# Performance work log

Measured on AMD Instinct MI355X. Metric: run time of the kernel, lower is better.

## Reference

```python
import jax, jax.numpy as jnp
import numpy as np

B, N, D, H = 8, 1024, 768, 12
HD = D // H


def setup_inputs() -> dict:
    key = jax.random.key(0)
    ks = jax.random.split(key, 9)
    s = 1.0 / np.sqrt(D)
    return {
        "x": jax.random.normal(ks[0], (B, N, D), dtype=jnp.float32),
        "Wq": jax.random.normal(ks[1], (D, D), dtype=jnp.float32) * s,
        "bq": jax.random.normal(ks[2], (D,), dtype=jnp.float32) * 0.01,
        "Wk": jax.random.normal(ks[3], (D, D), dtype=jnp.float32) * s,
        "bk": jax.random.normal(ks[4], (D,), dtype=jnp.float32) * 0.01,
        "Wv": jax.random.normal(ks[5], (D, D), dtype=jnp.float32) * s,
        "bv": jax.random.normal(ks[6], (D,), dtype=jnp.float32) * 0.01,
        "Wo": jax.random.normal(ks[7], (D, D), dtype=jnp.float32) * s,
        "bo": jax.random.normal(ks[8], (D,), dtype=jnp.float32) * 0.01,
    }


def reference(x, Wq, bq, Wk, bk, Wv, bv, Wo, bo):
    b, n, d = x.shape
    split = lambda t: t.reshape(b, n, H, HD).transpose(0, 2, 1, 3)  # b h n d
    q = split(x @ Wq + bq)
    k = split(x @ Wk + bk)
    v = split(x @ Wv + bv)
    energy = jnp.einsum('bhqd,bhkd->bhqk', q, k)
    # NOTE: module scales AFTER softmax by sqrt(emb_size) (not head_dim) -- faithful.
    att = jax.nn.softmax(energy, axis=-1) / jnp.sqrt(jnp.float32(D)).astype(x.dtype)
    out = jnp.einsum('bhqk,bhkd->bhqd', att, v)
    out = out.transpose(0, 2, 1, 3).reshape(b, n, d)
    return out @ Wo + bo
```

## Files before the change

kernel.cpp:

```cpp
#include <hip/hip_runtime.h>

#define B_  8
#define N_  1024
#define D_  768
#define H_  12
#define HD_ 64
#define M_  (B_ * N_)
#define WELEM (D_ * D_)
#define XELEM ((size_t)M_ * D_)

typedef _Float16 f16;
typedef f16   f16x8  __attribute__((ext_vector_type(8)));
typedef short bf16x8 __attribute__((ext_vector_type(8)));
typedef float f32x4  __attribute__((ext_vector_type(4)));
typedef unsigned short u16;

__device__ __forceinline__ u16 f2bf(float f) {
    unsigned int x = __float_as_uint(f);
    return (u16)((x + 0x7fffu + ((x >> 16) & 1u)) >> 16);
}
__device__ __forceinline__ u16 f2h(float f) {
    return __builtin_bit_cast(u16, (f16)f);
}
__device__ __forceinline__ unsigned int cvtpk_bf16(float lo, float hi) {
    unsigned int r;
    asm("v_cvt_pk_bf16_f32 %0, %1, %2" : "=v"(r) : "v"(lo), "v"(hi));
    return r;
}
#if __has_builtin(__builtin_amdgcn_exp2f)
#define EXP2F(x) __builtin_amdgcn_exp2f(x)
#else
#define EXP2F(x) exp2f(x)
#endif

#define LOG2E_   1.4426950408889634f
#define EXPBIAS_ 28.853900817779268f

typedef __attribute__((address_space(3))) unsigned int       as3_u32;
typedef __attribute__((address_space(1))) const unsigned int as1_u32;
__device__ __forceinline__ void dma16(const void* g, void* l) {
    __builtin_amdgcn_global_load_lds((as1_u32*)g, (as3_u32*)l, 16, 0, 0);
}

__global__ __launch_bounds__(256) void cvt_x(const float* __restrict__ X,
                                             u16* __restrict__ Xh) {
    int idx = blockIdx.x * 256 + threadIdx.x;
    float4 v = ((const float4*)X)[idx];
    ushort4 o = {f2h(v.x), f2h(v.y), f2h(v.z), f2h(v.w)};
    ((ushort4*)Xh)[idx] = o;
}

__global__ __launch_bounds__(256) void cvt_w(
    const float* __restrict__ w0, const float* __restrict__ w1,
    const float* __restrict__ w2, const float* __restrict__ w3,
    u16* __restrict__ Wt) {
    const float* W = blockIdx.y == 0 ? w0 : blockIdx.y == 1 ? w1
                   : blockIdx.y == 2 ? w2 : w3;
    u16* dst = Wt + (size_t)blockIdx.y * WELEM;
    const int t  = threadIdx.x;
    const int tk = (blockIdx.x % 12) * 64, tn = (blockIdx.x / 12) * 64;
    __shared__ __align__(16) float tile[64][68];
#pragma unroll
    for (int i = 0; i < 4; ++i) {
        int r = (t >> 4) + i * 16, c4 = (t & 15) * 4;
        float4 v = *(const float4*)(W + (size_t)(tk + r) * D_ + tn + c4);
        *(float4*)&tile[r][c4] = v;
    }
    __syncthreads();
#pragma unroll
    for (int i = 0; i < 4; ++i) {
        int nr = (t >> 4) + i * 16, kc = (t & 15) * 4;
        ushort4 o = {f2h(tile[kc + 0][nr]), f2h(tile[kc + 1][nr]),
                     f2h(tile[kc + 2][nr]), f2h(tile[kc + 3][nr])};
        *(ushort4*)(dst + (size_t)(tn + nr) * D_ + tk + kc) = o;
    }
}

__global__ __launch_bounds__(256, 3) void gemm_qkv(
    const u16* __restrict__ Xh, const u16* __restrict__ Wt,
    const float* __restrict__ bq, const float* __restrict__ bk,
    const float* __restrict__ bv, u16* __restrict__ Qf,
    u16* __restrict__ Kf, u16* __restrict__ Vt) {
    __shared__ __align__(16) u16 As[128 * 64];
    __shared__ __align__(16) u16 Bs[3 * 64 * 64];

    const int id  = blockIdx.x;
    const int xcd = id & 7, idx = id >> 3;
    const int m0  = (xcd * 8 + idx / 12) * 128;
    const int n0  = (idx % 12) * 64;

    const int t = threadIdx.x, lane = t & 63, w = t >> 6;
    const int wm = w >> 1, wn = w & 1;
    const int quad = lane >> 4, ln = lane & 15;
    const int drow = lane >> 3, dcl = (lane & 7) ^ ((lane >> 3) & 7);

    f32x4 acc[3][4][2] = {};
    for (int k0 = 0; k0 < D_; k0 += 64) {
        __syncthreads();
#pragma unroll
        for (int j = 0; j < 4; ++j) {
            int i = w * 4 + j, row = i * 8 + drow;
            dma16(Xh + (size_t)(m0 + row) * D_ + k0 + dcl * 8, &As[i * 512]);
        }
#pragma unroll
        for (int z = 0; z < 3; ++z)
#pragma unroll
            for (int j = 0; j < 2; ++j) {
                int i = w * 2 + j, row = i * 8 + drow;
                dma16(Wt + (size_t)z * WELEM + (size_t)(n0 + row) * D_ + k0 + dcl * 8,
                      &Bs[z * 4096 + i * 512]);
            }
        __syncthreads();
        f16x8 a[4][2];
#pragma unroll
        for (int mt = 0; mt < 4; ++mt)
#pragma unroll
            for (int ks = 0; ks < 2; ++ks)
                a[mt][ks] = *(const f16x8*)&As[(wm * 64 + mt * 16 + ln) * 64 +
                                               (((ks * 4 + quad) ^ (ln & 7)) * 8)];
#pragma unroll
        for (int z = 0; z < 3; ++z) {
            f16x8 b[2][2];
#pragma unroll
            for (int nt = 0; nt < 2; ++nt)
#pragma unroll
                for (int ks = 0; ks < 2; ++ks)
                    b[nt][ks] = *(const f16x8*)&Bs[z * 4096 +
                                                   (wn * 32 + nt * 16 + ln) * 64 +
                                                   (((ks * 4 + quad) ^ (ln & 7)) * 8)];
#pragma unroll
            for (int mt = 0; mt < 4; ++mt)
#pragma unroll
                for (int nt = 0; nt < 2; ++nt) {
                    acc[z][mt][nt] = __builtin_amdgcn_mfma_f32_16x16x32_f16(
                        a[mt][0], b[nt][0], acc[z][mt][nt], 0, 0, 0);
                    acc[z][mt][nt] = __builtin_amdgcn_mfma_f32_16x16x32_f16(
                        a[mt][1], b[nt][1], acc[z][mt][nt], 0, 0, 0);
                }
        }
    }
    const int h = n0 >> 6;
#pragma unroll
    for (int nt = 0; nt < 2; ++nt) {
        int hd = wn * 32 + nt * 16 + ln;
        float bq_ = bq[n0 + hd], bk_ = bk[n0 + hd], bv_ = bv[n0 + hd];
#pragma unroll
        for (int mt = 0; mt < 4; ++mt) {
            int mb = m0 + wm * 64 + mt * 16 + quad * 4;
            int bb = mb >> 10, ns = mb & 1023;
#pragma unroll
            for (int r = 0; r < 4; ++r)
                Qf[(((size_t)bb * H_ + h) * N_ + ns + r) * HD_ + hd] =
                    f2h((acc[0][mt][nt][r] + bq_) * LOG2E_);
#pragma unroll
            for (int r = 0; r < 4; ++r)
                Kf[(((size_t)bb * H_ + h) * N_ + ns + r) * HD_ + hd] =
                    f2h(acc[1][mt][nt][r] + bk_);
            ushort4 o = {f2bf(acc[2][mt][nt][0] + bv_), f2bf(acc[2][mt][nt][1] + bv_),
                         f2bf(acc[2][mt][nt][2] + bv_), f2bf(acc[2][mt][nt][3] + bv_)};
            *(ushort4*)(Vt + (((size_t)bb * H_ + h) * HD_ + hd) * N_ + ns) = o;
        }
    }
}

__global__ __launch_bounds__(512, 6) void attn_mfma(
    const u16* __restrict__ Qg, const u16* __restrict__ Kg,
    const u16* __restrict__ Vtg, u16* __restrict__ Og) {
    __shared__ __align__(16) u16 Ks[2][64 * 64];
    __shared__ __align__(16) u16 Vs[2][64 * 64];
    __shared__ __align__(16) u16 Ps[128 * 72];

    const int t = threadIdx.x, lane = t & 63, w = t >> 6;
    const int quad = lane >> 4, ln = lane & 15;
    const int drow = lane >> 3, dcl = (lane & 7) ^ ((lane >> 3) & 7);
    const int id  = blockIdx.x;
    const int id2 = (id & 7) * 96 + (id >> 3);
    const int bh  = id2 >> 3, qt = id2 & 7;
    const u16* Qh  = Qg  + ((size_t)bh * N_ + qt * 128) * HD_;
    const u16* Kh  = Kg  + (size_t)bh * N_ * HD_;
    const u16* Vth = Vtg + (size_t)bh * HD_ * N_;
    u16*       Oh  = Og  + ((size_t)bh * N_ + qt * 128) * HD_;

    const int rho = w * 8 + drow;
    const int gk  = 4 * (rho & 15) + (rho >> 4);

    f16x8 aq[2];
#pragma unroll
    for (int ks = 0; ks < 2; ++ks)
        aq[ks] = *(const f16x8*)(Qh + (size_t)(w * 16 + ln) * HD_ +
                                 ks * 32 + quad * 8);

    const bf16x8 pone = {0x3F80, 0x3F80, 0x3F80, 0x3F80,
                         0x3F80, 0x3F80, 0x3F80, 0x3F80};
    const f32x4 nb = {-EXPBIAS_, -EXPBIAS_, -EXPBIAS_, -EXPBIAS_};

    f32x4 oacc[4] = {};
    f32x4 lacc = {};

    dma16(Kh + (size_t)gk * HD_ + dcl * 8, &Ks[0][w * 512]);
    dma16(Vth + (size_t)rho * N_ + dcl * 8, &Vs[0][w * 512]);

#pragma unroll 2
    for (int kt = 0; kt < 16; ++kt) {
        const int cur = kt & 1;
        if (kt < 15) {
            const int nk = (kt + 1) * 64;
            dma16(Kh + (size_t)(nk + gk) * HD_ + dcl * 8, &Ks[cur ^ 1][w * 512]);
            dma16(Vth + (size_t)rho * N_ + nk + dcl * 8, &Vs[cur ^ 1][w * 512]);
            asm volatile("s_waitcnt vmcnt(2)" ::: "memory");
        } else {
            asm volatile("s_waitcnt vmcnt(0)" ::: "memory");
        }
        __builtin_amdgcn_s_barrier();
        __builtin_amdgcn_sched_barrier(0);

        f32x4 sf[4];
        __builtin_amdgcn_s_setprio(1);
#pragma unroll
        for (int nt = 0; nt < 4; ++nt) {
            f16x8 b0 = *(const f16x8*)&Ks[cur][(nt * 16 + ln) * 64 + ((quad) ^ (ln & 7)) * 8];
            f16x8 b1 = *(const f16x8*)&Ks[cur][(nt * 16 + ln) * 64 + ((4 + quad) ^ (ln & 7)) * 8];
            sf[nt] = __builtin_amdgcn_mfma_f32_16x16x32_f16(aq[0], b0, nb, 0, 0, 0);
            sf[nt] = __builtin_amdgcn_mfma_f32_16x16x32_f16(aq[1], b1, sf[nt], 0, 0, 0);
        }
        __builtin_amdgcn_s_setprio(0);

#pragma unroll
        for (int r = 0; r < 4; ++r) {
            float e0 = EXP2F(sf[0][r]);
            float e1 = EXP2F(sf[1][r]);
            float e2 = EXP2F(sf[2][r]);
            float e3 = EXP2F(sf[3][r]);
            uint2 pk;
            pk.x = cvtpk_bf16(e0, e1);
            pk.y = cvtpk_bf16(e2, e3);
            int q = w * 16 + quad * 4 + r;
            *(uint2*)&Ps[q * 72 + ln * 4] = pk;
        }

        __builtin_amdgcn_s_setprio(1);
        {
            bf16x8 ap0 = *(const bf16x8*)&Ps[(w * 16 + ln) * 72 + quad * 8];
            bf16x8 ap1 = *(const bf16x8*)&Ps[(w * 16 + ln) * 72 + 32 + quad * 8];
            lacc = __builtin_amdgcn_mfma_f32_16x16x32_bf16(ap0, pone, lacc, 0, 0, 0);
            lacc = __builtin_amdgcn_mfma_f32_16x16x32_bf16(ap1, pone, lacc, 0, 0, 0);
#pragma unroll
            for (int nt = 0; nt < 4; ++nt) {
                bf16x8 bv0 = *(const bf16x8*)&Vs[cur][(nt * 16 + ln) * 64 +
                                                      ((quad ^ (ln & 7)) * 8)];
                oacc[nt] = __builtin_amdgcn_mfma_f32_16x16x32_bf16(
                    ap0, bv0, oacc[nt], 0, 0, 0);
                bf16x8 bv1 = *(const bf16x8*)&Vs[cur][(nt * 16 + ln) * 64 +
                                                      (((4 + quad) ^ (ln & 7)) * 8)];
                oacc[nt] = __builtin_amdgcn_mfma_f32_16x16x32_bf16(
                    ap1, bv1, oacc[nt], 0, 0, 0);
            }
        }
        __builtin_amdgcn_s_setprio(0);
        __builtin_amdgcn_sched_barrier(0);
        __builtin_amdgcn_s_barrier();
    }

    const float sc = 0.036084391824351615f;
#pragma unroll
    for (int r = 0; r < 4; ++r) {
        float inv = sc / lacc[r];
#pragma unroll
        for (int nt = 0; nt < 4; ++nt)
            Oh[(size_t)(w * 16 + quad * 4 + r) * HD_ + nt * 16 + ln] =
                f2h(oacc[nt][r] * inv);
    }
}

__global__ __launch_bounds__(256) void gemm_out(
    const u16* __restrict__ Ob, const u16* __restrict__ Wto,
    const float* __restrict__ bias, float* __restrict__ Out) {
    __shared__ __align__(16) u16 As[128 * 64];
    __shared__ __align__(16) u16 Bs[64 * 64];

    const int id  = blockIdx.x;
    const int id2 = (id & 7) * 96 + (id >> 3);
    const int m0  = (id2 / 12) * 128, n0 = (id2 % 12) * 64;

    const int t = threadIdx.x, lane = t & 63, w = t >> 6;
    const int wm = w >> 1, wn = w & 1;
    const int quad = lane >> 4, ln = lane & 15;
    const int drow = lane >> 3, dcl = (lane & 7) ^ ((lane >> 3) & 7);

    f32x4 acc[4][2] = {};
    for (int k0 = 0; k0 < D_; k0 += 64) {
        int head = k0 >> 6;
        __syncthreads();
#pragma unroll
        for (int j = 0; j < 4; ++j) {
            int i = w * 4 + j, row = i * 8 + drow;
            int m = m0 + row, bb = m >> 10, ns = m & 1023;
            dma16(Ob + (((size_t)bb * H_ + head) * N_ + ns) * HD_ + dcl * 8, &As[i * 512]);
        }
#pragma unroll
        for (int j = 0; j < 2; ++j) {
            int i = w * 2 + j, row = i * 8 + drow;
            dma16(Wto + (size_t)(n0 + row) * D_ + k0 + dcl * 8, &Bs[i * 512]);
        }
        __syncthreads();
        f16x8 a[4][2], b[2][2];
#pragma unroll
        for (int mt = 0; mt < 4; ++mt)
#pragma unroll
            for (int ks = 0; ks < 2; ++ks)
                a[mt][ks] = *(const f16x8*)&As[(wm * 64 + mt * 16 + ln) * 64 +
                                               (((ks * 4 + quad) ^ (ln & 7)) * 8)];
#pragma unroll
        for (int nt = 0; nt < 2; ++nt)
#pragma unroll
            for (int ks = 0; ks < 2; ++ks)
                b[nt][ks] = *(const f16x8*)&Bs[(wn * 32 + nt * 16 + ln) * 64 +
                                               (((ks * 4 + quad) ^ (ln & 7)) * 8)];
#pragma unroll
        for (int mt = 0; mt < 4; ++mt)
#pragma unroll
            for (int nt = 0; nt < 2; ++nt) {
                acc[mt][nt] = __builtin_amdgcn_mfma_f32_16x16x32_f16(
                    a[mt][0], b[nt][0], acc[mt][nt], 0, 0, 0);
                acc[mt][nt] = __builtin_amdgcn_mfma_f32_16x16x32_f16(
                    a[mt][1], b[nt][1], acc[mt][nt], 0, 0, 0);
            }
    }
#pragma unroll
    for (int nt = 0; nt < 2; ++nt) {
        int n = n0 + wn * 32 + nt * 16 + ln;
        float bv_ = bias[n];
#pragma unroll
        for (int mt = 0; mt < 4; ++mt) {
            int mb = m0 + wm * 64 + mt * 16 + quad * 4;
#pragma unroll
            for (int r = 0; r < 4; ++r)
                Out[(size_t)(mb + r) * D_ + n] = acc[mt][nt][r] + bv_;
        }
    }
}

extern "C" void kernel_launch(void* const* d_in, const int* in_sizes, int n_in,
                              void* d_out, int out_size, void* d_ws, size_t ws_size,
                              hipStream_t stream) {
    const float* x  = (const float*)d_in[0];
    const float* Wq = (const float*)d_in[1];
    const float* bq = (const float*)d_in[2];
    const float* Wk = (const float*)d_in[3];
    const float* bk = (const float*)d_in[4];
    const float* Wv = (const float*)d_in[5];
    const float* bv = (const float*)d_in[6];
    const float* Wo = (const float*)d_in[7];
    const float* bo = (const float*)d_in[8];

    u16* Xh = (u16*)d_ws;
    u16* Wt = Xh + XELEM;
    u16* Qf = Wt + 4 * (size_t)WELEM;
    u16* Kf = Qf + XELEM;
    u16* Vt = Kf + XELEM;
    u16* Ob = Vt + XELEM;

    cvt_x<<<dim3((int)(XELEM / 4 / 256)), 256, 0, stream>>>(x, Xh);
    cvt_w<<<dim3(144, 4), 256, 0, stream>>>(Wq, Wk, Wv, Wo, Wt);
    gemm_qkv<<<dim3(768), 256, 0, stream>>>(Xh, Wt, bq, bk, bv, Qf, Kf, Vt);
    attn_mfma<<<dim3(768), 512, 0, stream>>>(Qf, Kf, Vt, Ob);
    gemm_out<<<dim3(768), 256, 0, stream>>>(
        Ob, Wt + 3 * (size_t)WELEM, bo, (float*)d_out);
}
```

Measured before the change: 183.5 us.

## Double attention query tile per block to reuse K/V tiles across more rows

Each attention block now handles 256 query rows instead of 128, with each wave computing two 16-row M-tiles that share the same K and V fragments loaded from LDS. This halves the grid to 384 blocks and halves the total K/V global traffic and LDS B-operand reads per query. The cost is more registers, a larger P staging buffer, a lower occupancy hint (4 instead of 6 blocks), and fewer blocks than CUs' worth of parallel slots, which may leave the GPU underfilled.

```diff
diff --git a/kernel.cpp b/kernel.cpp
--- a/kernel.cpp
+++ b/kernel.cpp
@@ -163,39 +163,41 @@
     }
 }
 
-__global__ __launch_bounds__(512, 6) void attn_mfma(
+__global__ __launch_bounds__(512, 4) void attn_mfma(
     const u16* __restrict__ Qg, const u16* __restrict__ Kg,
     const u16* __restrict__ Vtg, u16* __restrict__ Og) {
     __shared__ __align__(16) u16 Ks[2][64 * 64];
     __shared__ __align__(16) u16 Vs[2][64 * 64];
-    __shared__ __align__(16) u16 Ps[128 * 72];
+    __shared__ __align__(16) u16 Ps[256 * 72];
 
     const int t = threadIdx.x, lane = t & 63, w = t >> 6;
     const int quad = lane >> 4, ln = lane & 15;
     const int drow = lane >> 3, dcl = (lane & 7) ^ ((lane >> 3) & 7);
     const int id  = blockIdx.x;
-    const int id2 = (id & 7) * 96 + (id >> 3);
-    const int bh  = id2 >> 3, qt = id2 & 7;
-    const u16* Qh  = Qg  + ((size_t)bh * N_ + qt * 128) * HD_;
+    const int id2 = (id & 7) * 48 + (id >> 3);
+    const int bh  = id2 >> 2, qt = id2 & 3;
+    const u16* Qh  = Qg  + ((size_t)bh * N_ + qt * 256) * HD_;
     const u16* Kh  = Kg  + (size_t)bh * N_ * HD_;
     const u16* Vth = Vtg + (size_t)bh * HD_ * N_;
-    u16*       Oh  = Og  + ((size_t)bh * N_ + qt * 128) * HD_;
+    u16*       Oh  = Og  + ((size_t)bh * N_ + qt * 256) * HD_;
 
     const int rho = w * 8 + drow;
     const int gk  = 4 * (rho & 15) + (rho >> 4);
 
-    f16x8 aq[2];
-#pragma unroll
-    for (int ks = 0; ks < 2; ++ks)
-        aq[ks] = *(const f16x8*)(Qh + (size_t)(w * 16 + ln) * HD_ +
-                                 ks * 32 + quad * 8);
+    f16x8 aq[2][2];
+#pragma unroll
+    for (int mt = 0; mt < 2; ++mt)
+#pragma unroll
+        for (int ks = 0; ks < 2; ++ks)
+            aq[mt][ks] = *(const f16x8*)(Qh + (size_t)(w * 32 + mt * 16 + ln) * HD_ +
+                                         ks * 32 + quad * 8);
 
     const bf16x8 pone = {0x3F80, 0x3F80, 0x3F80, 0x3F80,
                          0x3F80, 0x3F80, 0x3F80, 0x3F80};
     const f32x4 nb = {-EXPBIAS_, -EXPBIAS_, -EXPBIAS_, -EXPBIAS_};
 
-    f32x4 oacc[4] = {};
-    f32x4 lacc = {};
+    f32x4 oacc[2][4] = {};
+    f32x4 lacc[2] = {};
 
     dma16(Kh + (size_t)gk * HD_ + dcl * 8, &Ks[0][w * 512]);
     dma16(Vth + (size_t)rho * N_ + dcl * 8, &Vs[0][w * 512]);
@@ -214,46 +216,58 @@
         __builtin_amdgcn_s_barrier();
         __builtin_amdgcn_sched_barrier(0);
 
-        f32x4 sf[4];
+        f32x4 sf[2][4];
         __builtin_amdgcn_s_setprio(1);
 #pragma unroll
         for (int nt = 0; nt < 4; ++nt) {
             f16x8 b0 = *(const f16x8*)&Ks[cur][(nt * 16 + ln) * 64 + ((quad) ^ (ln & 7)) * 8];
             f16x8 b1 = *(const f16x8*)&Ks[cur][(nt * 16 + ln) * 64 + ((4 + quad) ^ (ln & 7)) * 8];
-            sf[nt] = __builtin_amdgcn_mfma_f32_16x16x32_f16(aq[0], b0, nb, 0, 0, 0);
-            sf[nt] = __builtin_amdgcn_mfma_f32_16x16x32_f16(aq[1], b1, sf[nt], 0, 0, 0);
+#pragma unroll
+            for (int mt = 0; mt < 2; ++mt) {
+                sf[mt][nt] = __builtin_amdgcn_mfma_f32_16x16x32_f16(aq[mt][0], b0, nb, 0, 0, 0);
+                sf[mt][nt] = __builtin_amdgcn_mfma_f32_16x16x32_f16(aq[mt][1], b1, sf[mt][nt], 0, 0, 0);
+            }
         }
         __builtin_amdgcn_s_setprio(0);
 
 #pragma unroll
-        for (int r = 0; r < 4; ++r) {
-            float e0 = EXP2F(sf[0][r]);
-            float e1 = EXP2F(sf[1][r]);
-            float e2 = EXP2F(sf[2][r]);
-            float e3 = EXP2F(sf[3][r]);
-            uint2 pk;
-            pk.x = cvtpk_bf16(e0, e1);
-            pk.y = cvtpk_bf16(e2, e3);
-            int q = w * 16 + quad * 4 + r;
-            *(uint2*)&Ps[q * 72 + ln * 4] = pk;
-        }
+        for (int mt = 0; mt < 2; ++mt)
+#pragma unroll
+            for (int r = 0; r < 4; ++r) {
+                float e0 = EXP2F(sf[mt][0][r]);
+                float e1 = EXP2F(sf[mt][1][r]);
+                float e2 = EXP2F(sf[mt][2][r]);
+                float e3 = EXP2F(sf[mt][3][r]);
+                uint2 pk;
+                pk.x = cvtpk_bf16(e0, e1);
+                pk.y = cvtpk_bf16(e2, e3);
+                int q = w * 32 + mt * 16 + quad * 4 + r;
+                *(uint2*)&Ps[q * 72 + ln * 4] = pk;
+            }
 
         __builtin_amdgcn_s_setprio(1);
         {
-            bf16x8 ap0 = *(const bf16x8*)&Ps[(w * 16 + ln) * 72 + quad * 8];
-            bf16x8 ap1 = *(const bf16x8*)&Ps[(w * 16 + ln) * 72 + 32 + quad * 8];
-            lacc = __builtin_amdgcn_mfma_f32_16x16x32_bf16(ap0, pone, lacc, 0, 0, 0);
-            lacc = __builtin_amdgcn_mfma_f32_16x16x32_bf16(ap1, pone, lacc, 0, 0, 0);
+            bf16x8 ap0[2], ap1[2];
+#pragma unroll
+            for (int mt = 0; mt < 2; ++mt) {
+                ap0[mt] = *(const bf16x8*)&Ps[(w * 32 + mt * 16 + ln) * 72 + quad * 8];
+                ap1[mt] = *(const bf16x8*)&Ps[(w * 32 + mt * 16 + ln) * 72 + 32 + quad * 8];
+                lacc[mt] = __builtin_amdgcn_mfma_f32_16x16x32_bf16(ap0[mt], pone, lacc[mt], 0, 0, 0);
+                lacc[mt] = __builtin_amdgcn_mfma_f32_16x16x32_bf16(ap1[mt], pone, lacc[mt], 0, 0, 0);
+            }
 #pragma unroll
             for (int nt = 0; nt < 4; ++nt) {
                 bf16x8 bv0 = *(const bf16x8*)&Vs[cur][(nt * 16 + ln) * 64 +
                                                       ((quad ^ (ln & 7)) * 8)];
-                oacc[nt] = __builtin_amdgcn_mfma_f32_16x16x32_bf16(
-                    ap0, bv0, oacc[nt], 0, 0, 0);
                 bf16x8 bv1 = *(const bf16x8*)&Vs[cur][(nt * 16 + ln) * 64 +
                                                       (((4 + quad) ^ (ln & 7)) * 8)];
-                oacc[nt] = __builtin_amdgcn_mfma_f32_16x16x32_bf16(
-                    ap1, bv1, oacc[nt], 0, 0, 0);
+#pragma unroll
+                for (int mt = 0; mt < 2; ++mt) {
+                    oacc[mt][nt] = __builtin_amdgcn_mfma_f32_16x16x32_bf16(
+                        ap0[mt], bv0, oacc[mt][nt], 0, 0, 0);
+                    oacc[mt][nt] = __builtin_amdgcn_mfma_f32_16x16x32_bf16(
+                        ap1[mt], bv1, oacc[mt][nt], 0, 0, 0);
+                }
             }
         }
         __builtin_amdgcn_s_setprio(0);
@@ -263,13 +277,15 @@
 
     const float sc = 0.036084391824351615f;
 #pragma unroll
-    for (int r = 0; r < 4; ++r) {
-        float inv = sc / lacc[r];
-#pragma unroll
-        for (int nt = 0; nt < 4; ++nt)
-            Oh[(size_t)(w * 16 + quad * 4 + r) * HD_ + nt * 16 + ln] =
-                f2h(oacc[nt][r] * inv);
-    }
+    for (int mt = 0; mt < 2; ++mt)
+#pragma unroll
+        for (int r = 0; r < 4; ++r) {
+            float inv = sc / lacc[mt][r];
+#pragma unroll
+            for (int nt = 0; nt < 4; ++nt)
+                Oh[(size_t)(w * 32 + mt * 16 + quad * 4 + r) * HD_ + nt * 16 + ln] =
+                    f2h(oacc[mt][nt][r] * inv);
+        }
 }
 
 __global__ __launch_bounds__(256) void gemm_out(
@@ -363,7 +379,7 @@
     cvt_x<<<dim3((int)(XELEM / 4 / 256)), 256, 0, stream>>>(x, Xh);
     cvt_w<<<dim3(144, 4), 256, 0, stream>>>(Wq, Wk, Wv, Wo, Wt);
     gemm_qkv<<<dim3(768), 256, 0, stream>>>(Xh, Wt, bq, bk, bv, Qf, Kf, Vt);
-    attn_mfma<<<dim3(768), 512, 0, stream>>>(Qf, Kf, Vt, Ob);
+    attn_mfma<<<dim3(384), 512, 0, stream>>>(Qf, Kf, Vt, Ob);
     gemm_out<<<dim3(768), 256, 0, stream>>>(
         Ob, Wt + 3 * (size_t)WELEM, bo, (float*)d_out);
 }
```

After: 179.7 us. 1.02x faster.
